# Kernel tuning notes

Measured on AMD Instinct MI355X. Metric: run time of the kernel, lower is better.

The kernel has to match this reference:

```python
import jax, jax.numpy as jnp
import numpy as np
from jax.scipy.special import gammaln, logsumexp

T, BATCH = 500, 64
S, A, OBS, CTL, H = 64, 16, 32, 8, 30


def _scale_tril(lv, tl):
    # lv [K,D], tl [K,D,D] -> lower-triangular L with exp(lv) on the diagonal
    D = lv.shape[-1]
    return jnp.tril(tl, -1) + jnp.exp(lv)[..., None] * jnp.eye(D, dtype=lv.dtype)


def mvn_logprob(x, mu, lv, tl):
    # x [T,B,D], mixture of K full-cov MVNs (mu [K,D]) -> logp [T,B,K]
    D = mu.shape[-1]
    L = _scale_tril(lv, tl)  # [K,D,D]
    eye = jnp.eye(D, dtype=x.dtype)
    Linv = jax.vmap(lambda l: jax.scipy.linalg.solve_triangular(l, eye, lower=True))(L)
    diff = x[:, :, None, :] - mu  # [T,B,K,D] (dominant intermediate)
    z = jnp.einsum('kij,tbkj->tbki', Linv, diff)
    return -0.5 * jnp.sum(z * z, -1) - jnp.sum(lv, -1) - 0.5 * D * jnp.log(2.0 * jnp.pi)


def reference(o, u, obs_mu, obs_lv, obs_tl, ctl_mu, ctl_lv, ctl_tl, B_logits, D_logits, C_logits, tau):
    logp_o = mvn_logprob(o, obs_mu, obs_lv, obs_tl)  # [T,B,S]
    logp_u = mvn_logprob(u, ctl_mu, ctl_lv, ctl_tl)  # [T,B,A]
    p_a = jax.nn.softmax(logp_u, -1)
    Bp = jax.nn.softmax(B_logits, -1)  # [A,S,S] transition probs
    b0 = jnp.broadcast_to(jax.nn.softmax(D_logits, -1), logp_o.shape[1:])  # [B,S]

    def hmm_step(b, inp):
        lo, pa = inp  # [B,S], [B,A]
        prior = jnp.einsum('na,asj,ns->nj', pa, Bp, b)  # action-averaged predict
        lik = jnp.exp(lo - jnp.max(lo, -1, keepdims=True))  # stable, normalization cancels
        post = lik * prior
        bn = post / jnp.sum(post, -1, keepdims=True)
        return bn, bn

    _, b_seq = jax.lax.scan(hmm_step, b0, (logp_o, p_a))
    b = jnp.concatenate([b0[None], b_seq])  # [T+1,B,S]

    # reward R = -KL(B || C) - obs entropy (literal torch: sum(B*logB - logC, -1))
    obs_ent = 0.5 * OBS * (1.0 + jnp.log(2.0 * jnp.pi)) + jnp.sum(obs_lv, -1)  # [S]
    Cp = jax.nn.softmax(C_logits, -1)  # [S]
    kl = jnp.sum(Bp * jnp.log(Bp) - jnp.log(Cp), -1)  # [A,S]
    R = -kl - obs_ent[None, :]  # [A,S]

    def vi_step(Q, _):
        V = logsumexp(Q, axis=0)  # soft-max over actions -> [S]
        Qn = R + jnp.einsum('asj,j->as', Bp, V)
        return Qn, Qn

    _, Qs = jax.lax.scan(vi_step, R, None, length=H - 1)
    Qh = jnp.concatenate([R[None], Qs])  # [H,A,S]

    rate = jnp.exp(tau[0, 0])
    k = jnp.arange(H, dtype=o.dtype)
    logh = k * jnp.log(rate) - rate - gammaln(k + 1.0)
    h = jax.nn.softmax(logh)  # normalized (truncated) Poisson horizon pdf
    Q = jnp.einsum('h,has->as', h, Qh)  # [A,S]

    G = jnp.einsum('tns,as->tna', b[:-1], Q)  # expected free energy per action
    logp_pi = logsumexp(jax.nn.log_softmax(G, -1) + logp_u, -1)  # [T,B]
    logp_b = jnp.log(b[1:] + 1e-6)
    logp_obs = logsumexp(logp_b * logp_o, -1)  # [T,B] (literal to torch source)
    return logp_pi, logp_obs


def setup_inputs() -> dict:
    key = jax.random.key(0)
    ks = jax.random.split(key, 12)
    f = jnp.float32
    return {
        'o': jax.random.normal(ks[0], (T, BATCH, OBS), f),
        'u': jax.random.normal(ks[1], (T, BATCH, CTL), f),
        'obs_mu': jax.random.normal(ks[2], (S, OBS), f),
        'obs_lv': 0.1 * jax.random.normal(ks[3], (S, OBS), f),
        'obs_tl': 0.1 * jax.random.normal(ks[4], (S, OBS, OBS), f),
        'ctl_mu': jax.random.normal(ks[5], (A, CTL), f),
        'ctl_lv': 0.1 * jax.random.normal(ks[6], (A, CTL), f),
        'ctl_tl': 0.1 * jax.random.normal(ks[7], (A, CTL, CTL), f),
        'B_logits': jax.random.normal(ks[8], (A, S, S), f),
        'D_logits': jax.random.normal(ks[9], (S,), f),
        'C_logits': jax.random.normal(ks[10], (S,), f),
        'tau': 0.5 * jax.random.normal(ks[11], (1, 1), f),
    }
```

## Files before the change

kernel.cpp:

```cpp
#include <hip/hip_runtime.h>
#include <math.h>

#define T_STEPS 500
#define BATCH   64
#define S_DIM   64
#define A_DIM   16
#define OBS_D   32
#define CTL_D   8
#define H_DIM   30

#define CHUNKS   8
#define CHUNK_L  63
#define BURN     31
#define MAXSTEPS (CHUNK_L + BURN)

#define LOG2PI 1.8378770664093453f

typedef _Float16 v2h __attribute__((ext_vector_type(2)));
typedef __fp16  fp16x2 __attribute__((ext_vector_type(2)));

__device__ __forceinline__ float wmax(float v){
  #pragma unroll
  for (int o = 32; o > 0; o >>= 1) v = fmaxf(v, __shfl_xor(v, o, 64));
  return v;
}
__device__ __forceinline__ float wsum(float v){
  #pragma unroll
  for (int o = 32; o > 0; o >>= 1) v += __shfl_xor(v, o, 64);
  return v;
}

template<int CTRL>
__device__ __forceinline__ float dpp_add(float v){
  int x = __builtin_amdgcn_update_dpp(0, __float_as_int(v), CTRL, 0xF, 0xF, true);
  return v + __int_as_float(x);
}
__device__ __forceinline__ v2h u2h(unsigned int x){
  union { unsigned int u; v2h h; } c; c.u = x; return c.h;
}
__device__ __forceinline__ unsigned int pack_pkrtz(float a, float b){
  union { fp16x2 h; unsigned int u; } c;
  c.h = __builtin_amdgcn_cvt_pkrtz(a, b);
  return c.u;
}

#define BAR() do { \
  asm volatile("s_waitcnt lgkmcnt(0)" ::: "memory"); \
  __builtin_amdgcn_s_barrier(); \
  asm volatile("" ::: "memory"); \
  __builtin_amdgcn_sched_barrier(0); \
} while (0)

#define FOR16(X) X(0) X(1) X(2) X(3) X(4) X(5) X(6) X(7) X(8) X(9) X(10) X(11) X(12) X(13) X(14) X(15)

__global__ __launch_bounds__(256) void k_front(const float* __restrict__ o,
                                               const float* __restrict__ obs_mu,
                                               const float* __restrict__ obs_lv,
                                               const float* __restrict__ obs_tl,
                                               const float* __restrict__ Blog,
                                               const float* __restrict__ u,
                                               const float* __restrict__ ctl_mu,
                                               const float* __restrict__ ctl_lv,
                                               const float* __restrict__ ctl_tl,
                                               float* __restrict__ lo_out,
                                               _Float16* __restrict__ Bph,
                                               float* __restrict__ lup,
                                               float* __restrict__ pap){
  const int bx  = blockIdx.x;
  const int tid = threadIdx.x;

  if (bx < 8000){
    const int k = bx & 63;
    const float* __restrict__ Lk  = obs_tl + k * OBS_D * OBS_D;
    const float* __restrict__ muk = obs_mu + k * OBS_D;
    const float* __restrict__ lvk = obs_lv + k * OBS_D;

    float dinv[OBS_D];
    float lvsum = 0.f;
    #pragma unroll
    for (int i = 0; i < OBS_D; ++i){
      float x = lvk[i];
      lvsum += x;
      dinv[i] = __expf(-x);
    }

    const int item = (bx >> 6) * 256 + tid;
    const float* op = o + item * OBS_D;
    float d[OBS_D];
    #pragma unroll
    for (int i = 0; i < OBS_D; i += 4){
      float4 v = *(const float4*)(op + i);
      d[i]   = v.x - muk[i];
      d[i+1] = v.y - muk[i+1];
      d[i+2] = v.z - muk[i+2];
      d[i+3] = v.w - muk[i+3];
    }
    float z[OBS_D];
    float acc = 0.f;
    #pragma unroll
    for (int i = 0; i < OBS_D; ++i){
      float s0 = d[i], s1 = 0.f;
      #pragma unroll
      for (int jj = 0; jj + 1 < i; jj += 2){
        s0 = fmaf(-Lk[i * OBS_D + jj],     z[jj],     s0);
        s1 = fmaf(-Lk[i * OBS_D + jj + 1], z[jj + 1], s1);
      }
      if (i & 1) s0 = fmaf(-Lk[i * OBS_D + i - 1], z[i - 1], s0);
      float zz = (s0 + s1) * dinv[i];
      z[i] = zz;
      acc  = fmaf(zz, zz, acc);
    }
    lo_out[item * S_DIM + k] = -0.5f * acc - lvsum - 0.5f * OBS_D * LOG2PI;
    return;
  }

  if (bx < 8256){
    const int row  = (bx - 8000) * 4 + (tid >> 6);
    const int lane = tid & 63;
    float v = Blog[row * 64 + lane];
    float m = wmax(v);
    float e = __expf(v - m);
    float s = wsum(e);
    const int a  = row >> 6;
    const int ss = row & 63;
    Bph[(a * 64 + lane) * 64 + ss] = (_Float16)(e / s);
    return;
  }

  const int item = (bx - 8256) * 256 + tid;
  const float* up = u + item * CTL_D;
  float uu[CTL_D];
  #pragma unroll
  for (int i = 0; i < CTL_D; i += 4){
    float4 v = *(const float4*)(up + i);
    uu[i] = v.x; uu[i+1] = v.y; uu[i+2] = v.z; uu[i+3] = v.w;
  }
  float lp[A_DIM];
  #pragma unroll
  for (int a = 0; a < A_DIM; ++a){
    float z[CTL_D];
    float acc = 0.f, lvs = 0.f;
    #pragma unroll
    for (int i = 0; i < CTL_D; ++i){
      float lvv = ctl_lv[a * CTL_D + i];
      lvs += lvv;
      float s = uu[i] - ctl_mu[a * CTL_D + i];
      #pragma unroll
      for (int jj = 0; jj < i; ++jj) s = fmaf(-ctl_tl[a * 64 + i * CTL_D + jj], z[jj], s);
      z[i] = s * __expf(-lvv);
      acc  = fmaf(z[i], z[i], acc);
    }
    lp[a] = -0.5f * acc - lvs - 0.5f * CTL_D * LOG2PI;
  }
  float m = -1e30f;
  #pragma unroll
  for (int a = 0; a < A_DIM; ++a) m = fmaxf(m, lp[a]);
  float e[A_DIM], se = 0.f;
  #pragma unroll
  for (int a = 0; a < A_DIM; ++a){ e[a] = __expf(lp[a] - m); se += e[a]; }
  float inv = 1.f / se;
  #pragma unroll
  for (int a = 0; a < A_DIM; ++a){
    lup[item * A_DIM + a] = lp[a];
    pap[item * A_DIM + a] = e[a] * inv;
  }
}

__global__ __launch_bounds__(1024, 1) void k_vi(const float* __restrict__ Blog,
                                                const float* __restrict__ obs_lv,
                                                const float* __restrict__ Clog,
                                                const float* __restrict__ tau,
                                                float* __restrict__ Qout){
  const int tid  = threadIdx.x;
  const int lane = tid & 63;
  __shared__ __align__(16) float Vs[S_DIM];
  __shared__ __align__(16) float Qlds[A_DIM][S_DIM];
  __shared__ float hs[H_DIM];

  float c  = Clog[lane];
  float cm = wmax(c);
  float cs = wsum(__expf(c - cm));
  float lseC = cm + __logf(cs);
  float sumLnCp = wsum(c) - 64.f * lseC;

  if (tid < 64){
    float t0   = tau[0];
    float rate = __expf(t0);
    float lg = 0.f;
    for (int i = 2; i <= lane; ++i) lg += __logf((float)i);
    float lh = (lane < H_DIM) ? ((float)lane * t0 - rate - lg) : -1e30f;
    float m  = wmax(lh);
    float e  = (lane < H_DIM) ? __expf(lh - m) : 0.f;
    float s  = wsum(e);
    if (lane < H_DIM) hs[lane] = e / s;
  }

  const int r = tid;
  const int a = r >> 6, s = r & 63;
  const float* p = Blog + r * 64;
  float4 raw[16];
  float mr = -1e30f;
  #pragma unroll
  for (int q = 0; q < 16; ++q){
    float4 v = *(const float4*)(p + 4 * q);
    raw[q] = v;
    mr = fmaxf(mr, fmaxf(fmaxf(v.x, v.y), fmaxf(v.z, v.w)));
  }
  float ssum = 0.f, dot = 0.f;
  #pragma unroll
  for (int q = 0; q < 16; ++q){
    float4 v = raw[q];
    float4 e;
    e.x = __expf(v.x - mr); e.y = __expf(v.y - mr);
    e.z = __expf(v.z - mr); e.w = __expf(v.w - mr);
    ssum += (e.x + e.y) + (e.z + e.w);
    dot  += e.x * (v.x - mr) + e.y * (v.y - mr) + e.z * (v.z - mr) + e.w * (v.w - mr);
    raw[q] = e;
  }
  float inv = 1.f / ssum;
  float lns = __logf(ssum);
  #pragma unroll
  for (int q = 0; q < 16; ++q){
    float4 e = raw[q];
    raw[q] = make_float4(e.x * inv, e.y * inv, e.z * inv, e.w * inv);
  }
  float negent = dot * inv - lns;

  float oe = 0.f;
  const float* lvp = obs_lv + s * OBS_D;
  #pragma unroll
  for (int dd = 0; dd < OBS_D; dd += 4){
    float4 v = *(const float4*)(lvp + dd);
    oe += v.x + v.y + v.z + v.w;
  }
  oe += 0.5f * OBS_D * (1.f + LOG2PI);
  float R  = -negent + sumLnCp - oe;
  float Qc = R;
  __syncthreads();
  float Qa = hs[0] * R;

  for (int it = 1; it < H_DIM; ++it){
    Qlds[a][s] = Qc;
    __syncthreads();
    if (tid < 64){
      float m = -1e30f;
      #pragma unroll
      for (int aa = 0; aa < A_DIM; ++aa) m = fmaxf(m, Qlds[aa][lane]);
      float sv = 0.f;
      #pragma unroll
      for (int aa = 0; aa < A_DIM; ++aa) sv += __expf(Qlds[aa][lane] - m);
      Vs[lane] = m + __logf(sv);
    }
    __syncthreads();
    float hw = hs[it];
    float accA = 0.f, accB = 0.f;
    #pragma unroll
    for (int q = 0; q < 16; ++q){
      float4 v = *(const float4*)(&Vs[4 * q]);
      accA = fmaf(raw[q].x, v.x, fmaf(raw[q].y, v.y, accA));
      accB = fmaf(raw[q].z, v.z, fmaf(raw[q].w, v.w, accB));
    }
    Qc = R + accA + accB;
    Qa = fmaf(hw, Qc, Qa);
  }
  Qout[r] = Qa;
}

__global__ __launch_bounds__(512, 4)
void k_scan(const _Float16* __restrict__ Bph,
            const float* __restrict__ lo,
            const float* __restrict__ pa,
            const float* __restrict__ Dlog,
            float* __restrict__ bseq){
  const int n   = blockIdx.x;
  const int c   = blockIdx.y;
  const int tid = threadIdx.x;
  const int g   = tid >> 6;
  const int l   = tid & 63;
  const int so  = l & 7;
  const int jj  = l >> 3;
  const int j   = g * 8 + jj;

  const int t_out0  = c * CHUNK_L;
  const int t_end   = (t_out0 + CHUNK_L < T_STEPS) ? (t_out0 + CHUNK_L) : T_STEPS;
  const int t_start = (c == 0) ? 0 : (t_out0 - BURN);
  const int nsteps  = t_end - t_start;

  __shared__ __align__(16) float lik_lds[MAXSTEPS][S_DIM];
  __shared__ __align__(16) unsigned int b16[2][32];
  __shared__ __align__(16) unsigned short ps16[2][8];

  #define DECLT(A) uint4 Tq##A;
  FOR16(DECLT)
  #define LOADT(A) Tq##A = *(const uint4*)(Bph + ((A) * 4096 + j * 64 + 8 * so));
  FOR16(LOADT)
  #define PINT(A) asm volatile("" : "+v"(Tq##A.x), "+v"(Tq##A.y), "+v"(Tq##A.z), "+v"(Tq##A.w));
  FOR16(PINT)

  const float* lo_n = lo + n * 64;
  const float* pa_n = pa + n * 16;
  for (int i = tid; i < nsteps * 64; i += 512){
    int r = i >> 6, col = i & 63;
    lik_lds[r][col] = lo_n[(t_start + r) * 4096 + col];
  }
  if (tid < 64){
    float dl = (c == 0) ? Dlog[l] : 0.f;
    float m = wmax(dl);
    float e = __expf(dl - m);
    float s = wsum(e);
    float b0 = e / s;
    if (c == 0) bseq[n * 64 + l] = b0;
    float nb = __shfl_xor(b0, 1, 64);
    if (!(l & 1)) b16[0][l >> 1] = pack_pkrtz(b0, nb);
  }
  if (tid < 8) ps16[0][tid] = 0x3000;
  __syncthreads();

  for (int r = g; r < nsteps; r += 8){
    float v = lik_lds[r][l];
    float m = wmax(v);
    lik_lds[r][l] = __expf(v - m);
  }
  __syncthreads();

  #define DECLPA(A) float pac_##A, pan_##A;
  FOR16(DECLPA)
  const float* pp0 = pa_n + t_start * 1024;
  #define LDPA0(A) pac_##A = pp0[A];
  FOR16(LDPA0)

  int cur = 0;
  for (int tt = 0; tt < nsteps; ++tt){
    const int t   = t_start + tt;
    const int nxt = cur ^ 1;

    const int t1 = (t + 1 < T_STEPS) ? (t + 1) : (T_STEPS - 1);
    const float* pp1 = pa_n + t1 * 1024;
    #define LDPAN(A) pan_##A = pp1[A];
    FOR16(LDPAN)

    float likr = lik_lds[tt][j];
    uint4 q = *(const uint4*)&ps16[cur][0];
    v2h a01 = u2h(q.x) + u2h(q.y);
    v2h a23 = u2h(q.z) + u2h(q.w);
    v2h aa  = a01 + a23;
    float sum = (float)aa.x + (float)aa.y;
    float lik = likr * __builtin_amdgcn_rcpf(sum);

    uint4 bq = *(const uint4*)&b16[cur][so * 4];
    v2h bh0 = u2h(bq.x), bh1 = u2h(bq.y), bh2 = u2h(bq.z), bh3 = u2h(bq.w);

    float pr0 = 0.f, pr1 = 0.f, pr2 = 0.f, pr3 = 0.f;
    #define DOTQ(A, P) { \
      float y = __builtin_amdgcn_fdot2(u2h(Tq##A.x), bh0, \
                __builtin_amdgcn_fdot2(u2h(Tq##A.y), bh1, \
                __builtin_amdgcn_fdot2(u2h(Tq##A.z), bh2, \
                __builtin_amdgcn_fdot2(u2h(Tq##A.w), bh3, 0.f, false), false), false), false); \
      P = fmaf(pac_##A, y, P); }
    DOTQ(0,  pr0) DOTQ(1,  pr1) DOTQ(2,  pr2) DOTQ(3,  pr3)
    DOTQ(4,  pr0) DOTQ(5,  pr1) DOTQ(6,  pr2) DOTQ(7,  pr3)
    DOTQ(8,  pr0) DOTQ(9,  pr1) DOTQ(10, pr2) DOTQ(11, pr3)
    DOTQ(12, pr0) DOTQ(13, pr1) DOTQ(14, pr2) DOTQ(15, pr3)
    float pri = (pr0 + pr1) + (pr2 + pr3);

    pri = dpp_add<0xB1>(pri);
    pri = dpp_add<0x4E>(pri);
    pri = dpp_add<0x141>(pri);

    float post = pri * lik;
    if (t >= t_out0){
      if (so == 0)
        bseq[(t + 1) * 4096 + n * 64 + j] = post;
    }

    {
      int x = __builtin_amdgcn_update_dpp(0, __float_as_int(post), 0x128, 0xF, 0xF, true);
      if (!(l & 15)) b16[nxt][g * 4 + (l >> 4)] = pack_pkrtz(post, __int_as_float(x));
    }

    {
      float w = post;
      w = dpp_add<0x128>(w);
      w = dpp_add<0x142>(w);
      w = dpp_add<0x143>(w);
      if (l == 48) ps16[nxt][g] = (unsigned short)(pack_pkrtz(w, 0.f) & 0xffffu);
    }

    #define CPPA(A) pac_##A = pan_##A;
    FOR16(CPPA)

    BAR();
    cur = nxt;
  }
}

__global__ __launch_bounds__(256, 1) void k_out(const float* __restrict__ bseq,
                                                const float* __restrict__ Qg,
                                                const float* __restrict__ lo,
                                                const float* __restrict__ lu,
                                                float* __restrict__ out){
  __shared__ __align__(16) float Qs[A_DIM][S_DIM];
  const int tid = threadIdx.x;
  for (int i = tid; i < A_DIM * S_DIM; i += 256) Qs[i >> 6][i & 63] = Qg[i];
  __syncthreads();

  const int item = blockIdx.x * 256 + tid;
  float bs[64];
  const float* bp_ = bseq + item * 64;
  float bsum = 0.f;
  #pragma unroll
  for (int i = 0; i < 16; ++i){
    float4 v = *(const float4*)(bp_ + 4 * i);
    bs[4*i] = v.x; bs[4*i+1] = v.y; bs[4*i+2] = v.z; bs[4*i+3] = v.w;
    bsum += (v.x + v.y) + (v.z + v.w);
  }
  float binv = 1.0f / bsum;

  float G[A_DIM];
  #pragma unroll
  for (int a = 0; a < A_DIM; ++a){
    float acc = 0.f;
    #pragma unroll
    for (int s = 0; s < 64; ++s) acc = fmaf(bs[s], Qs[a][s], acc);
    G[a] = acc * binv;
  }
  const float* lup = lu + item * A_DIM;
  float m1 = -1e30f, m0 = -1e30f;
  float x1[A_DIM];
  #pragma unroll
  for (int a = 0; a < A_DIM; ++a){
    x1[a] = G[a] + lup[a];
    m1 = fmaxf(m1, x1[a]);
    m0 = fmaxf(m0, G[a]);
  }
  float e1 = 0.f, e0 = 0.f;
  #pragma unroll
  for (int a = 0; a < A_DIM; ++a){
    e1 += __expf(x1[a] - m1);
    e0 += __expf(G[a] - m0);
  }
  out[item] = (m1 + __logf(e1)) - (m0 + __logf(e0));

  const float* bq = bseq + (item + 64) * 64;
  float bsum2 = 0.f;
  #pragma unroll
  for (int i = 0; i < 16; ++i){
    float4 v = *(const float4*)(bq + 4 * i);
    bs[4*i] = v.x; bs[4*i+1] = v.y; bs[4*i+2] = v.z; bs[4*i+3] = v.w;
    bsum2 += (v.x + v.y) + (v.z + v.w);
  }
  float inv2 = 1.0f / bsum2;
  const float* lop = lo + item * 64;
  float terms[64];
  float mt = -1e30f;
  #pragma unroll
  for (int i = 0; i < 16; ++i){
    float4 v = *(const float4*)(lop + 4 * i);
    float t0 = __logf(bs[4*i]   * inv2 + 1e-6f) * v.x;
    float t1 = __logf(bs[4*i+1] * inv2 + 1e-6f) * v.y;
    float t2 = __logf(bs[4*i+2] * inv2 + 1e-6f) * v.z;
    float t3 = __logf(bs[4*i+3] * inv2 + 1e-6f) * v.w;
    terms[4*i] = t0; terms[4*i+1] = t1; terms[4*i+2] = t2; terms[4*i+3] = t3;
    mt = fmaxf(mt, fmaxf(fmaxf(t0, t1), fmaxf(t2, t3)));
  }
  float es = 0.f;
  #pragma unroll
  for (int s = 0; s < 64; ++s) es += __expf(terms[s] - mt);
  out[T_STEPS * BATCH + item] = mt + __logf(es);
}

extern "C" void kernel_launch(void* const* d_in, const int* in_sizes, int n_in,
                              void* d_out, int out_size, void* d_ws, size_t ws_size,
                              hipStream_t stream){
  const float* o      = (const float*)d_in[0];
  const float* u      = (const float*)d_in[1];
  const float* obs_mu = (const float*)d_in[2];
  const float* obs_lv = (const float*)d_in[3];
  const float* obs_tl = (const float*)d_in[4];
  const float* ctl_mu = (const float*)d_in[5];
  const float* ctl_lv = (const float*)d_in[6];
  const float* ctl_tl = (const float*)d_in[7];
  const float* Blog   = (const float*)d_in[8];
  const float* Dlog   = (const float*)d_in[9];
  const float* Clog   = (const float*)d_in[10];
  const float* tau    = (const float*)d_in[11];
  float* out = (float*)d_out;
  float* ws  = (float*)d_ws;

  _Float16* Bph = (_Float16*)ws;
  float* Q    = ws + 32768;
  float* lo   = ws + 33792;
  float* lu   = ws + 2081792;
  float* pa   = ws + 2593792;
  float* bseq = ws + 3105792;

  k_front<<<8381, 256, 0, stream>>>(o, obs_mu, obs_lv, obs_tl, Blog,
                                    u, ctl_mu, ctl_lv, ctl_tl, lo, Bph, lu, pa);
  k_vi   <<<1, 1024, 0, stream>>>(Blog, obs_lv, Clog, tau, Q);
  k_scan <<<dim3(64, CHUNKS), 512, 0, stream>>>(Bph, lo, pa, Dlog, bseq);
  k_out  <<<125, 256, 0, stream>>>(bseq, Q, lo, lu, out);
}
```

Before: 211.9 us.

## Transpose obs log-likelihood layout and split HMM scan into more chunks

The observation log-likelihood buffer is stored state-major ([S][T*B]), so k_front writes it coalesced across items and k_out reads it coalesced per state. The chunked HMM scan doubles the chunk count with shorter chunks and a burn-in of 30 steps, which shortens the serial critical path and doubles the number of blocks. In exchange, k_scan's loads into LDS become strided gathers, more burn-in work is repeated relative to the output steps, and the shorter burn-in may slightly change numerical agreement.

```diff
diff --git a/kernel.cpp b/kernel.cpp
--- a/kernel.cpp
+++ b/kernel.cpp
@@ -9,10 +9,11 @@
 #define CTL_D   8
 #define H_DIM   30
 
-#define CHUNKS   8
-#define CHUNK_L  63
-#define BURN     31
+#define CHUNKS   16
+#define CHUNK_L  32
+#define BURN     30
 #define MAXSTEPS (CHUNK_L + BURN)
+#define NITEMS   32000
 
 #define LOG2PI 1.8378770664093453f
 
@@ -62,7 +63,7 @@
                                                const float* __restrict__ ctl_mu,
                                                const float* __restrict__ ctl_lv,
                                                const float* __restrict__ ctl_tl,
-                                               float* __restrict__ lo_out,
+                                               float* __restrict__ lo_t,
                                                _Float16* __restrict__ Bph,
                                                float* __restrict__ lup,
                                                float* __restrict__ pap){
@@ -110,7 +111,7 @@
       z[i] = zz;
       acc  = fmaf(zz, zz, acc);
     }
-    lo_out[item * S_DIM + k] = -0.5f * acc - lvsum - 0.5f * OBS_D * LOG2PI;
+    lo_t[k * NITEMS + item] = -0.5f * acc - lvsum - 0.5f * OBS_D * LOG2PI;
     return;
   }
 
@@ -268,7 +269,7 @@
 
 __global__ __launch_bounds__(512, 4)
 void k_scan(const _Float16* __restrict__ Bph,
-            const float* __restrict__ lo,
+            const float* __restrict__ lo_t,
             const float* __restrict__ pa,
             const float* __restrict__ Dlog,
             float* __restrict__ bseq){
@@ -297,11 +298,10 @@
   #define PINT(A) asm volatile("" : "+v"(Tq##A.x), "+v"(Tq##A.y), "+v"(Tq##A.z), "+v"(Tq##A.w));
   FOR16(PINT)
 
-  const float* lo_n = lo + n * 64;
   const float* pa_n = pa + n * 16;
   for (int i = tid; i < nsteps * 64; i += 512){
     int r = i >> 6, col = i & 63;
-    lik_lds[r][col] = lo_n[(t_start + r) * 4096 + col];
+    lik_lds[r][col] = lo_t[col * NITEMS + (t_start + r) * 64 + n];
   }
   if (tid < 64){
     float dl = (c == 0) ? Dlog[l] : 0.f;
@@ -396,7 +396,7 @@
 
 __global__ __launch_bounds__(256, 1) void k_out(const float* __restrict__ bseq,
                                                 const float* __restrict__ Qg,
-                                                const float* __restrict__ lo,
+                                                const float* __restrict__ lo_t,
                                                 const float* __restrict__ lu,
                                                 float* __restrict__ out){
   __shared__ __align__(16) float Qs[A_DIM][S_DIM];
@@ -450,18 +450,15 @@
     bsum2 += (v.x + v.y) + (v.z + v.w);
   }
   float inv2 = 1.0f / bsum2;
-  const float* lop = lo + item * 64;
+  const float* lot = lo_t + item;
   float terms[64];
   float mt = -1e30f;
   #pragma unroll
-  for (int i = 0; i < 16; ++i){
-    float4 v = *(const float4*)(lop + 4 * i);
-    float t0 = __logf(bs[4*i]   * inv2 + 1e-6f) * v.x;
-    float t1 = __logf(bs[4*i+1] * inv2 + 1e-6f) * v.y;
-    float t2 = __logf(bs[4*i+2] * inv2 + 1e-6f) * v.z;
-    float t3 = __logf(bs[4*i+3] * inv2 + 1e-6f) * v.w;
-    terms[4*i] = t0; terms[4*i+1] = t1; terms[4*i+2] = t2; terms[4*i+3] = t3;
-    mt = fmaxf(mt, fmaxf(fmaxf(t0, t1), fmaxf(t2, t3)));
+  for (int s = 0; s < 64; ++s){
+    float lov = lot[s * NITEMS];
+    float tm  = __logf(bs[s] * inv2 + 1e-6f) * lov;
+    terms[s] = tm;
+    mt = fmaxf(mt, tm);
   }
   float es = 0.f;
   #pragma unroll
@@ -489,14 +486,14 @@
 
   _Float16* Bph = (_Float16*)ws;
   float* Q    = ws + 32768;
-  float* lo   = ws + 33792;
+  float* lo_t = ws + 33792;
   float* lu   = ws + 2081792;
   float* pa   = ws + 2593792;
   float* bseq = ws + 3105792;
 
   k_front<<<8381, 256, 0, stream>>>(o, obs_mu, obs_lv, obs_tl, Blog,
-                                    u, ctl_mu, ctl_lv, ctl_tl, lo, Bph, lu, pa);
+                                    u, ctl_mu, ctl_lv, ctl_tl, lo_t, Bph, lu, pa);
   k_vi   <<<1, 1024, 0, stream>>>(Blog, obs_lv, Clog, tau, Q);
-  k_scan <<<dim3(64, CHUNKS), 512, 0, stream>>>(Bph, lo, pa, Dlog, bseq);
-  k_out  <<<125, 256, 0, stream>>>(bseq, Q, lo, lu, out);
-}
+  k_scan <<<dim3(64, CHUNKS), 512, 0, stream>>>(Bph, lo_t, pa, Dlog, bseq);
+  k_out  <<<125, 256, 0, stream>>>(bseq, Q, lo_t, lu, out);
+}
```

Result: slower. 238.6 us (+12.6%).
